# Optimization experiments

Hardware: AMD Instinct MI355X
Metric: run time of the kernel (lower is better)

The kernel has to match this reference:

```python
import jax, jax.numpy as jnp
import numpy as np

D_MODEL = 2048
N_HEADS = 32
N_KV = 8
D_K = D_MODEL // N_HEADS  # 64
N_REP = N_HEADS // N_KV   # 4


def setup_inputs() -> dict:
    key = jax.random.key(0)
    ks = jax.random.split(key, 5)
    B, T = 2, 2048
    s = 0.02
    return {
        "x": jax.random.normal(ks[0], (B, T, D_MODEL), dtype=jnp.float32),
        "Wq": jax.random.normal(ks[1], (D_MODEL, D_MODEL), dtype=jnp.float32) * s,
        "Wk": jax.random.normal(ks[2], (N_KV * D_K, D_MODEL), dtype=jnp.float32) * s,
        "Wv": jax.random.normal(ks[3], (N_KV * D_K, D_MODEL), dtype=jnp.float32) * s,
        "Wo": jax.random.normal(ks[4], (D_MODEL, D_MODEL), dtype=jnp.float32) * s,
    }


def reference(x, Wq, Wk, Wv, Wo):
    B, T, C = x.shape
    # projections (torch Linear: x @ W.T)
    Q = (x @ Wq.T).reshape(B, T, N_KV, N_REP, D_K)  # group query heads by kv group
    K = (x @ Wk.T).reshape(B, T, N_KV, D_K)
    V = (x @ Wv.T).reshape(B, T, N_KV, D_K)
    scale = 1.0 / jnp.sqrt(jnp.asarray(D_K, dtype=x.dtype))
    # scores: (B, n_kv, n_rep, T, T) == repeated-KV scores without materializing repeats
    scores = jnp.einsum('btgrd,bsgd->bgrts', Q, K) * scale
    causal_mask = jnp.triu(jnp.ones((T, T), dtype=bool), k=1)
    scores = jnp.where(causal_mask, -jnp.inf, scores)
    attn = jax.nn.softmax(scores, axis=-1)
    out = jnp.einsum('bgrts,bsgd->btgrd', attn, V).reshape(B, T, C)
    return out @ Wo.T
```

## Files before the change

kernel.cpp:

```cpp
#include <hip/hip_runtime.h>
#include <hip/hip_bf16.h>

typedef __attribute__((ext_vector_type(8))) short bf16x8;
typedef __attribute__((ext_vector_type(4))) float floatx4;

constexpr int D_MODEL = 2048;
constexpr int N_HEADS = 32;
constexpr int N_KV    = 8;
constexpr int B_      = 2;
constexpr int T_      = 2048;
constexpr int BT      = B_ * T_;
constexpr int NQKV    = 3072;

__device__ __forceinline__ unsigned short f2bf(float f) {
    __hip_bfloat16 h = __float2bfloat16(f);
    return *reinterpret_cast<unsigned short*>(&h);
}

__device__ __forceinline__ void gll16(const void* g, void* l) {
    typedef const __attribute__((address_space(1))) unsigned int* gp_t;
    typedef __attribute__((address_space(3))) unsigned int* lp_t;
    __builtin_amdgcn_global_load_lds((gp_t)g, (lp_t)l, 16, 0, 0);
}

__global__ __launch_bounds__(256) void cvt_all(
        const float* __restrict__ x,  const float* __restrict__ wq,
        const float* __restrict__ wk, const float* __restrict__ wv,
        unsigned short* __restrict__ dst) {
    size_t i4 = (size_t)blockIdx.x * 256 + threadIdx.x;
    size_t e = i4 * 4;
    const float* src; size_t off;
    if (e < 8388608)        { src = x;  off = 0; }
    else if (e < 12582912)  { src = wq; off = 8388608; }
    else if (e < 13631488)  { src = wk; off = 12582912; }
    else                    { src = wv; off = 13631488; }
    float4 f = *reinterpret_cast<const float4*>(src + (e - off));
    unsigned short u[4] = {f2bf(f.x), f2bf(f.y), f2bf(f.z), f2bf(f.w)};
    reinterpret_cast<uint2*>(dst)[i4] = *reinterpret_cast<const uint2*>(u);
}

__global__ __launch_bounds__(256) void cvt_bf16(
        const float* __restrict__ src, unsigned short* __restrict__ dst, int n4) {
    int i = blockIdx.x * 256 + threadIdx.x;
    if (i < n4) {
        float4 f = reinterpret_cast<const float4*>(src)[i];
        unsigned short u[4] = {f2bf(f.x), f2bf(f.y), f2bf(f.z), f2bf(f.w)};
        reinterpret_cast<uint2*>(dst)[i] = *reinterpret_cast<const uint2*>(u);
    }
}

template<bool C_F32>
__global__ __launch_bounds__(256) void gemm128(
        const unsigned short* __restrict__ A,
        const unsigned short* __restrict__ Bb,
        void* __restrict__ Cp,
        int M, int N, int K) {
    __shared__ unsigned short As[128 * 64];
    __shared__ unsigned short Bs[128 * 64];
    const int t = threadIdx.x;
    const int wave = t >> 6, lane = t & 63;
    const int l16 = lane & 15, quad = lane >> 4;
    const int wm = (wave & 1) * 64, wn = (wave >> 1) * 64;
    const int mtile = blockIdx.y * 128, ntile = blockIdx.x * 128;

    floatx4 acc[4][4] = {};

    for (int k0 = 0; k0 < K; k0 += 64) {
        __syncthreads();
#pragma unroll
        for (int c = 0; c < 4; c++) {
            int s = (c * 4 + wave) * 64 + lane;
            int row = s >> 3, k8 = (s & 7) ^ (row & 7);
            gll16(&A[(size_t)(mtile + row) * K + k0 + k8 * 8], &As[(c * 4 + wave) * 512]);
            gll16(&Bb[(size_t)(ntile + row) * K + k0 + k8 * 8], &Bs[(c * 4 + wave) * 512]);
        }
        __syncthreads();
#pragma unroll
        for (int kc = 0; kc < 2; kc++) {
            bf16x8 af[4], bfr[4];
#pragma unroll
            for (int i = 0; i < 4; i++) {
                int arow = wm + i * 16 + l16;
                af[i] = *reinterpret_cast<const bf16x8*>(
                    &As[(arow * 8 + ((kc * 4 + quad) ^ (arow & 7))) * 8]);
                int brow = wn + i * 16 + l16;
                bfr[i] = *reinterpret_cast<const bf16x8*>(
                    &Bs[(brow * 8 + ((kc * 4 + quad) ^ (brow & 7))) * 8]);
            }
#pragma unroll
            for (int i = 0; i < 4; i++)
#pragma unroll
                for (int jn = 0; jn < 4; jn++)
                    acc[i][jn] = __builtin_amdgcn_mfma_f32_16x16x32_bf16(
                        af[i], bfr[jn], acc[i][jn], 0, 0, 0);
        }
    }
#pragma unroll
    for (int i = 0; i < 4; i++)
#pragma unroll
        for (int jn = 0; jn < 4; jn++)
#pragma unroll
            for (int r = 0; r < 4; r++) {
                int row = mtile + wm + i * 16 + quad * 4 + r;
                int col = ntile + wn + jn * 16 + l16;
                if constexpr (C_F32)
                    ((float*)Cp)[(size_t)row * N + col] = acc[i][jn][r];
                else
                    ((unsigned short*)Cp)[(size_t)row * N + col] = f2bf(acc[i][jn][r]);
            }
}

__global__ __launch_bounds__(256) void vtrans(
        const unsigned short* __restrict__ QKV,
        unsigned short* __restrict__ Vt) {
    __shared__ unsigned short Ts[64][72];
    const int tb = blockIdx.x * 64;
    const int bg = blockIdx.y;
    const int b = bg >> 3, g = bg & 7;
    const int t = threadIdx.x;
#pragma unroll
    for (int it = 0; it < 2; it++) {
        int row = (t >> 3) + it * 32;
        int sl = t & 7;
        *reinterpret_cast<uint4*>(&Ts[row][sl * 8]) =
            *reinterpret_cast<const uint4*>(
                &QKV[(size_t)(b * T_ + tb + row) * NQKV + 2560 + g * 64 + sl * 8]);
    }
    __syncthreads();
#pragma unroll
    for (int it = 0; it < 2; it++) {
        int d = (t >> 3) + it * 32;
        int ks = t & 7;
        unsigned short u[8];
#pragma unroll
        for (int j = 0; j < 8; j++) u[j] = Ts[ks * 8 + j][d];
        *reinterpret_cast<uint4*>(&Vt[((size_t)bg * 64 + d) * T_ + tb + ks * 8]) =
            *reinterpret_cast<const uint4*>(u);
    }
}

__global__ __launch_bounds__(256) void attn3(
        const unsigned short* __restrict__ QKV,
        const unsigned short* __restrict__ Vt,
        unsigned short* __restrict__ O) {
    __shared__ unsigned short Ks[64 * 64];
    __shared__ unsigned short Vs[64 * 64];
    __shared__ unsigned short Ps[4][16 * 72];
    const int j  = blockIdx.x;
    const int bh = blockIdx.y;
    const int b = bh >> 5, h = bh & 31;
    const int g = h >> 2;
    const int t = threadIdx.x, wave = t >> 6, lane = t & 63;
    const int l16 = lane & 15, quad = lane >> 4;

    const int qtlA = j, qtlB = 31 - j;
    const int qA = qtlA * 64 + wave * 16 + l16;
    const int qB = qtlB * 64 + wave * 16 + l16;

    const unsigned short* qpA = QKV + (size_t)(b * T_ + qA) * NQKV + h * 64;
    const unsigned short* qpB = QKV + (size_t)(b * T_ + qB) * NQKV + h * 64;
    bf16x8 qA0 = *reinterpret_cast<const bf16x8*>(qpA + quad * 8);
    bf16x8 qA1 = *reinterpret_cast<const bf16x8*>(qpA + 32 + quad * 8);
    bf16x8 qB0 = *reinterpret_cast<const bf16x8*>(qpB + quad * 8);
    bf16x8 qB1 = *reinterpret_cast<const bf16x8*>(qpB + 32 + quad * 8);

    floatx4 oA[4] = {}, oB[4] = {};
    float lpA = 0.f, lpB = 0.f;

    for (int kt = 0; kt <= qtlB; kt++) {
        const int kb = kt * 64;
        const bool doA = (kt <= qtlA);
        __syncthreads();
#pragma unroll
        for (int c = 0; c < 2; c++) {
            int s = (c * 4 + wave) * 64 + lane;
            int row = s >> 3, k8 = (s & 7) ^ (row & 7);
            gll16(&QKV[(size_t)(b * T_ + kb + row) * NQKV + 2048 + g * 64 + k8 * 8],
                  &Ks[(c * 4 + wave) * 512]);
            gll16(&Vt[((size_t)(b * 8 + g) * 64 + row) * T_ + kb + k8 * 8],
                  &Vs[(c * 4 + wave) * 512]);
        }
        __syncthreads();

        floatx4 sA[4], sB[4];
#pragma unroll
        for (int nt = 0; nt < 4; nt++) {
            int krow = nt * 16 + l16;
            bf16x8 k0 = *reinterpret_cast<const bf16x8*>(
                &Ks[(krow * 8 + (quad ^ (krow & 7))) * 8]);
            bf16x8 k1 = *reinterpret_cast<const bf16x8*>(
                &Ks[(krow * 8 + ((4 + quad) ^ (krow & 7))) * 8]);
            floatx4 z = {};
            z = __builtin_amdgcn_mfma_f32_16x16x32_bf16(k0, qB0, z, 0, 0, 0);
            sB[nt] = __builtin_amdgcn_mfma_f32_16x16x32_bf16(k1, qB1, z, 0, 0, 0);
            if (doA) {
                floatx4 za = {};
                za = __builtin_amdgcn_mfma_f32_16x16x32_bf16(k0, qA0, za, 0, 0, 0);
                sA[nt] = __builtin_amdgcn_mfma_f32_16x16x32_bf16(k1, qA1, za, 0, 0, 0);
            }
        }

        const bool diagB = (kt == qtlB), diagA = (kt == qtlA);
#pragma unroll
        for (int nt = 0; nt < 4; nt++) {
            unsigned short u[4];
#pragma unroll
            for (int r = 0; r < 4; r++) {
                float p = __expf(sB[nt][r] * 0.125f);
                if (diagB && (kb + nt * 16 + quad * 4 + r) > qB) p = 0.f;
                lpB += p;
                u[r] = f2bf(p);
            }
            *reinterpret_cast<uint2*>(&Ps[wave][l16 * 72 + nt * 16 + quad * 4]) =
                *reinterpret_cast<const uint2*>(u);
        }
        {
            bf16x8 p0 = *reinterpret_cast<const bf16x8*>(&Ps[wave][l16 * 72 + quad * 8]);
            bf16x8 p1 = *reinterpret_cast<const bf16x8*>(&Ps[wave][l16 * 72 + 32 + quad * 8]);
#pragma unroll
            for (int dt = 0; dt < 4; dt++) {
                int vrow = dt * 16 + l16;
                bf16x8 v0 = *reinterpret_cast<const bf16x8*>(
                    &Vs[(vrow * 8 + (quad ^ (vrow & 7))) * 8]);
                bf16x8 v1 = *reinterpret_cast<const bf16x8*>(
                    &Vs[(vrow * 8 + ((4 + quad) ^ (vrow & 7))) * 8]);
                oB[dt] = __builtin_amdgcn_mfma_f32_16x16x32_bf16(p0, v0, oB[dt], 0, 0, 0);
                oB[dt] = __builtin_amdgcn_mfma_f32_16x16x32_bf16(p1, v1, oB[dt], 0, 0, 0);
            }
        }
        if (doA) {
#pragma unroll
            for (int nt = 0; nt < 4; nt++) {
                unsigned short u[4];
#pragma unroll
                for (int r = 0; r < 4; r++) {
                    float p = __expf(sA[nt][r] * 0.125f);
                    if (diagA && (kb + nt * 16 + quad * 4 + r) > qA) p = 0.f;
                    lpA += p;
                    u[r] = f2bf(p);
                }
                *reinterpret_cast<uint2*>(&Ps[wave][l16 * 72 + nt * 16 + quad * 4]) =
                    *reinterpret_cast<const uint2*>(u);
            }
            bf16x8 p0 = *reinterpret_cast<const bf16x8*>(&Ps[wave][l16 * 72 + quad * 8]);
            bf16x8 p1 = *reinterpret_cast<const bf16x8*>(&Ps[wave][l16 * 72 + 32 + quad * 8]);
#pragma unroll
            for (int dt = 0; dt < 4; dt++) {
                int vrow = dt * 16 + l16;
                bf16x8 v0 = *reinterpret_cast<const bf16x8*>(
                    &Vs[(vrow * 8 + (quad ^ (vrow & 7))) * 8]);
                bf16x8 v1 = *reinterpret_cast<const bf16x8*>(
                    &Vs[(vrow * 8 + ((4 + quad) ^ (vrow & 7))) * 8]);
                oA[dt] = __builtin_amdgcn_mfma_f32_16x16x32_bf16(p0, v0, oA[dt], 0, 0, 0);
                oA[dt] = __builtin_amdgcn_mfma_f32_16x16x32_bf16(p1, v1, oA[dt], 0, 0, 0);
            }
        }
    }

    lpA += __shfl_xor(lpA, 16); lpA += __shfl_xor(lpA, 32);
    lpB += __shfl_xor(lpB, 16); lpB += __shfl_xor(lpB, 32);
#pragma unroll
    for (int r = 0; r < 4; r++) {
        float invA = 1.0f / __shfl(lpA, quad * 4 + r);
        float invB = 1.0f / __shfl(lpB, quad * 4 + r);
        int rowA = b * T_ + qtlA * 64 + wave * 16 + quad * 4 + r;
        int rowB = b * T_ + qtlB * 64 + wave * 16 + quad * 4 + r;
#pragma unroll
        for (int dt = 0; dt < 4; dt++) {
            O[(size_t)rowA * D_MODEL + h * 64 + dt * 16 + l16] = f2bf(oA[dt][r] * invA);
            O[(size_t)rowB * D_MODEL + h * 64 + dt * 16 + l16] = f2bf(oB[dt][r] * invB);
        }
    }
}

extern "C" void kernel_launch(void* const* d_in, const int* in_sizes, int n_in,
                              void* d_out, int out_size, void* d_ws, size_t ws_size,
                              hipStream_t stream) {
    const float* x  = (const float*)d_in[0];
    const float* Wq = (const float*)d_in[1];
    const float* Wk = (const float*)d_in[2];
    const float* Wv = (const float*)d_in[3];
    const float* Wo = (const float*)d_in[4];

    unsigned short* xb   = (unsigned short*)d_ws;
    unsigned short* Wqkv = xb + (size_t)BT * D_MODEL;
    unsigned short* QKVo = Wqkv + (size_t)NQKV * D_MODEL;
    unsigned short* Vt   = QKVo + (size_t)BT * NQKV;
    unsigned short* Aw   = xb;
    unsigned short* Wob  = Wqkv;

    dim3 blk(256);
    cvt_all<<<dim3(14336), blk, 0, stream>>>(x, Wq, Wk, Wv, xb);
    gemm128<false><<<dim3(NQKV / 128, BT / 128), blk, 0, stream>>>(
        xb, Wqkv, QKVo, BT, NQKV, D_MODEL);
    cvt_bf16<<<dim3(D_MODEL * D_MODEL / 4 / 256), blk, 0, stream>>>(
        Wo, Wob, D_MODEL * D_MODEL / 4);
    vtrans<<<dim3(T_ / 64, B_ * N_KV), blk, 0, stream>>>(QKVo, Vt);
    attn3<<<dim3(16, B_ * N_HEADS), blk, 0, stream>>>(QKVo, Vt, Aw);
    gemm128<true><<<dim3(D_MODEL / 128, BT / 128), blk, 0, stream>>>(
        Aw, Wob, d_out, BT, D_MODEL, D_MODEL);
}
```

Measured before the change: 314.9 us.

## Fold softmax scale into Q projection, use exp2 and MFMA row sums

The QKV GEMM epilogue now multiplies the Q columns by 0.125*log2(e), so the attention kernel can call exp2 directly without a per-element multiply. The row-sum of probabilities is computed with an MFMA against a ones vector instead of scalar adds and shuffles. The attention loop now processes the two paired query tiles one after the other instead of interleaving them, and the causal mask check is limited to the diagonal tile. This cuts VALU work but loads the K/V tiles twice for the shared early key blocks, and Q is rounded to bf16 after scaling.

```diff
diff --git a/kernel.cpp b/kernel.cpp
--- a/kernel.cpp
+++ b/kernel.cpp
@@ -11,6 +11,8 @@
 constexpr int T_      = 2048;
 constexpr int BT      = B_ * T_;
 constexpr int NQKV    = 3072;
+
+constexpr float Q_SCALE = 0.18033688011112042f;
 
 __device__ __forceinline__ unsigned short f2bf(float f) {
     __hip_bfloat16 h = __float2bfloat16(f);
@@ -49,7 +51,7 @@
     }
 }
 
-template<bool C_F32>
+template<bool C_F32, bool SCALEQ>
 __global__ __launch_bounds__(256) void gemm128(
         const unsigned short* __restrict__ A,
         const unsigned short* __restrict__ Bb,
@@ -95,6 +97,7 @@
                         af[i], bfr[jn], acc[i][jn], 0, 0, 0);
         }
     }
+    float cscale = (SCALEQ && ntile < 2048) ? Q_SCALE : 1.0f;
 #pragma unroll
     for (int i = 0; i < 4; i++)
 #pragma unroll
@@ -106,7 +109,8 @@
                 if constexpr (C_F32)
                     ((float*)Cp)[(size_t)row * N + col] = acc[i][jn][r];
                 else
-                    ((unsigned short*)Cp)[(size_t)row * N + col] = f2bf(acc[i][jn][r]);
+                    ((unsigned short*)Cp)[(size_t)row * N + col] =
+                        f2bf(acc[i][jn][r] * cscale);
             }
 }
 
@@ -139,7 +143,7 @@
     }
 }
 
-__global__ __launch_bounds__(256) void attn3(
+__global__ __launch_bounds__(256) void attn4(
         const unsigned short* __restrict__ QKV,
         const unsigned short* __restrict__ Vt,
         unsigned short* __restrict__ O) {
@@ -153,70 +157,77 @@
     const int t = threadIdx.x, wave = t >> 6, lane = t & 63;
     const int l16 = lane & 15, quad = lane >> 4;
 
-    const int qtlA = j, qtlB = 31 - j;
-    const int qA = qtlA * 64 + wave * 16 + l16;
-    const int qB = qtlB * 64 + wave * 16 + l16;
-
-    const unsigned short* qpA = QKV + (size_t)(b * T_ + qA) * NQKV + h * 64;
-    const unsigned short* qpB = QKV + (size_t)(b * T_ + qB) * NQKV + h * 64;
-    bf16x8 qA0 = *reinterpret_cast<const bf16x8*>(qpA + quad * 8);
-    bf16x8 qA1 = *reinterpret_cast<const bf16x8*>(qpA + 32 + quad * 8);
-    bf16x8 qB0 = *reinterpret_cast<const bf16x8*>(qpB + quad * 8);
-    bf16x8 qB1 = *reinterpret_cast<const bf16x8*>(qpB + 32 + quad * 8);
-
-    floatx4 oA[4] = {}, oB[4] = {};
-    float lpA = 0.f, lpB = 0.f;
-
-    for (int kt = 0; kt <= qtlB; kt++) {
-        const int kb = kt * 64;
-        const bool doA = (kt <= qtlA);
-        __syncthreads();
-#pragma unroll
-        for (int c = 0; c < 2; c++) {
-            int s = (c * 4 + wave) * 64 + lane;
-            int row = s >> 3, k8 = (s & 7) ^ (row & 7);
-            gll16(&QKV[(size_t)(b * T_ + kb + row) * NQKV + 2048 + g * 64 + k8 * 8],
-                  &Ks[(c * 4 + wave) * 512]);
-            gll16(&Vt[((size_t)(b * 8 + g) * 64 + row) * T_ + kb + k8 * 8],
-                  &Vs[(c * 4 + wave) * 512]);
-        }
-        __syncthreads();
-
-        floatx4 sA[4], sB[4];
-#pragma unroll
-        for (int nt = 0; nt < 4; nt++) {
-            int krow = nt * 16 + l16;
-            bf16x8 k0 = *reinterpret_cast<const bf16x8*>(
-                &Ks[(krow * 8 + (quad ^ (krow & 7))) * 8]);
-            bf16x8 k1 = *reinterpret_cast<const bf16x8*>(
-                &Ks[(krow * 8 + ((4 + quad) ^ (krow & 7))) * 8]);
-            floatx4 z = {};
-            z = __builtin_amdgcn_mfma_f32_16x16x32_bf16(k0, qB0, z, 0, 0, 0);
-            sB[nt] = __builtin_amdgcn_mfma_f32_16x16x32_bf16(k1, qB1, z, 0, 0, 0);
-            if (doA) {
-                floatx4 za = {};
-                za = __builtin_amdgcn_mfma_f32_16x16x32_bf16(k0, qA0, za, 0, 0, 0);
-                sA[nt] = __builtin_amdgcn_mfma_f32_16x16x32_bf16(k1, qA1, za, 0, 0, 0);
-            }
-        }
-
-        const bool diagB = (kt == qtlB), diagA = (kt == qtlA);
-#pragma unroll
-        for (int nt = 0; nt < 4; nt++) {
-            unsigned short u[4];
-#pragma unroll
-            for (int r = 0; r < 4; r++) {
-                float p = __expf(sB[nt][r] * 0.125f);
-                if (diagB && (kb + nt * 16 + quad * 4 + r) > qB) p = 0.f;
-                lpB += p;
-                u[r] = f2bf(p);
-            }
-            *reinterpret_cast<uint2*>(&Ps[wave][l16 * 72 + nt * 16 + quad * 4]) =
-                *reinterpret_cast<const uint2*>(u);
-        }
-        {
+    bf16x8 ones;
+#pragma unroll
+    for (int i = 0; i < 8; i++) ones[i] = (short)0x3F80;
+
+    for (int pp = 0; pp < 2; pp++) {
+        const int qtl = pp ? (31 - j) : j;
+        const int qb0 = qtl * 64;
+        const int qq = qb0 + wave * 16 + l16;
+        const unsigned short* qptr = QKV + (size_t)(b * T_ + qq) * NQKV + h * 64;
+        bf16x8 qf0 = *reinterpret_cast<const bf16x8*>(qptr + quad * 8);
+        bf16x8 qf1 = *reinterpret_cast<const bf16x8*>(qptr + 32 + quad * 8);
+
+        floatx4 o[4] = {};
+        floatx4 lacc = {};
+
+        for (int kt = 0; kt <= qtl; kt++) {
+            const int kb = kt * 64;
+            __syncthreads();
+#pragma unroll
+            for (int c = 0; c < 2; c++) {
+                int s = (c * 4 + wave) * 64 + lane;
+                int row = s >> 3, k8 = (s & 7) ^ (row & 7);
+                gll16(&QKV[(size_t)(b * T_ + kb + row) * NQKV + 2048 + g * 64 + k8 * 8],
+                      &Ks[(c * 4 + wave) * 512]);
+                gll16(&Vt[((size_t)(b * 8 + g) * 64 + row) * T_ + kb + k8 * 8],
+                      &Vs[(c * 4 + wave) * 512]);
+            }
+            __syncthreads();
+
+            floatx4 sT[4];
+#pragma unroll
+            for (int nt = 0; nt < 4; nt++) {
+                int krow = nt * 16 + l16;
+                bf16x8 k0 = *reinterpret_cast<const bf16x8*>(
+                    &Ks[(krow * 8 + (quad ^ (krow & 7))) * 8]);
+                bf16x8 k1 = *reinterpret_cast<const bf16x8*>(
+                    &Ks[(krow * 8 + ((4 + quad) ^ (krow & 7))) * 8]);
+                floatx4 z = {};
+                z = __builtin_amdgcn_mfma_f32_16x16x32_bf16(k0, qf0, z, 0, 0, 0);
+                sT[nt] = __builtin_amdgcn_mfma_f32_16x16x32_bf16(k1, qf1, z, 0, 0, 0);
+            }
+
+            if (kt == qtl) {
+#pragma unroll
+                for (int nt = 0; nt < 4; nt++) {
+                    unsigned short u[4];
+#pragma unroll
+                    for (int r = 0; r < 4; r++) {
+                        float p = __builtin_amdgcn_exp2f(sT[nt][r]);
+                        if ((kb + nt * 16 + quad * 4 + r) > qq) p = 0.f;
+                        u[r] = f2bf(p);
+                    }
+                    *reinterpret_cast<uint2*>(&Ps[wave][l16 * 72 + nt * 16 + quad * 4]) =
+                        *reinterpret_cast<const uint2*>(u);
+                }
+            } else {
+#pragma unroll
+                for (int nt = 0; nt < 4; nt++) {
+                    unsigned short u[4];
+#pragma unroll
+                    for (int r = 0; r < 4; r++)
+                        u[r] = f2bf(__builtin_amdgcn_exp2f(sT[nt][r]));
+                    *reinterpret_cast<uint2*>(&Ps[wave][l16 * 72 + nt * 16 + quad * 4]) =
+                        *reinterpret_cast<const uint2*>(u);
+                }
+            }
+
             bf16x8 p0 = *reinterpret_cast<const bf16x8*>(&Ps[wave][l16 * 72 + quad * 8]);
             bf16x8 p1 = *reinterpret_cast<const bf16x8*>(&Ps[wave][l16 * 72 + 32 + quad * 8]);
+            lacc = __builtin_amdgcn_mfma_f32_16x16x32_bf16(p0, ones, lacc, 0, 0, 0);
+            lacc = __builtin_amdgcn_mfma_f32_16x16x32_bf16(p1, ones, lacc, 0, 0, 0);
 #pragma unroll
             for (int dt = 0; dt < 4; dt++) {
                 int vrow = dt * 16 + l16;
@@ -224,51 +235,18 @@
                     &Vs[(vrow * 8 + (quad ^ (vrow & 7))) * 8]);
                 bf16x8 v1 = *reinterpret_cast<const bf16x8*>(
                     &Vs[(vrow * 8 + ((4 + quad) ^ (vrow & 7))) * 8]);
-                oB[dt] = __builtin_amdgcn_mfma_f32_16x16x32_bf16(p0, v0, oB[dt], 0, 0, 0);
-                oB[dt] = __builtin_amdgcn_mfma_f32_16x16x32_bf16(p1, v1, oB[dt], 0, 0, 0);
-            }
-        }
-        if (doA) {
-#pragma unroll
-            for (int nt = 0; nt < 4; nt++) {
-                unsigned short u[4];
-#pragma unroll
-                for (int r = 0; r < 4; r++) {
-                    float p = __expf(sA[nt][r] * 0.125f);
-                    if (diagA && (kb + nt * 16 + quad * 4 + r) > qA) p = 0.f;
-                    lpA += p;
-                    u[r] = f2bf(p);
-                }
-                *reinterpret_cast<uint2*>(&Ps[wave][l16 * 72 + nt * 16 + quad * 4]) =
-                    *reinterpret_cast<const uint2*>(u);
-            }
-            bf16x8 p0 = *reinterpret_cast<const bf16x8*>(&Ps[wave][l16 * 72 + quad * 8]);
-            bf16x8 p1 = *reinterpret_cast<const bf16x8*>(&Ps[wave][l16 * 72 + 32 + quad * 8]);
-#pragma unroll
-            for (int dt = 0; dt < 4; dt++) {
-                int vrow = dt * 16 + l16;
-                bf16x8 v0 = *reinterpret_cast<const bf16x8*>(
-                    &Vs[(vrow * 8 + (quad ^ (vrow & 7))) * 8]);
-                bf16x8 v1 = *reinterpret_cast<const bf16x8*>(
-                    &Vs[(vrow * 8 + ((4 + quad) ^ (vrow & 7))) * 8]);
-                oA[dt] = __builtin_amdgcn_mfma_f32_16x16x32_bf16(p0, v0, oA[dt], 0, 0, 0);
-                oA[dt] = __builtin_amdgcn_mfma_f32_16x16x32_bf16(p1, v1, oA[dt], 0, 0, 0);
-            }
-        }
-    }
-
-    lpA += __shfl_xor(lpA, 16); lpA += __shfl_xor(lpA, 32);
-    lpB += __shfl_xor(lpB, 16); lpB += __shfl_xor(lpB, 32);
-#pragma unroll
-    for (int r = 0; r < 4; r++) {
-        float invA = 1.0f / __shfl(lpA, quad * 4 + r);
-        float invB = 1.0f / __shfl(lpB, quad * 4 + r);
-        int rowA = b * T_ + qtlA * 64 + wave * 16 + quad * 4 + r;
-        int rowB = b * T_ + qtlB * 64 + wave * 16 + quad * 4 + r;
-#pragma unroll
-        for (int dt = 0; dt < 4; dt++) {
-            O[(size_t)rowA * D_MODEL + h * 64 + dt * 16 + l16] = f2bf(oA[dt][r] * invA);
-            O[(size_t)rowB * D_MODEL + h * 64 + dt * 16 + l16] = f2bf(oB[dt][r] * invB);
+                o[dt] = __builtin_amdgcn_mfma_f32_16x16x32_bf16(p0, v0, o[dt], 0, 0, 0);
+                o[dt] = __builtin_amdgcn_mfma_f32_16x16x32_bf16(p1, v1, o[dt], 0, 0, 0);
+            }
+        }
+
+#pragma unroll
+        for (int r = 0; r < 4; r++) {
+            float inv = 1.0f / lacc[r];
+            int row = b * T_ + qb0 + wave * 16 + quad * 4 + r;
+#pragma unroll
+            for (int dt = 0; dt < 4; dt++)
+                O[(size_t)row * D_MODEL + h * 64 + dt * 16 + l16] = f2bf(o[dt][r] * inv);
         }
     }
 }
@@ -291,12 +269,12 @@
 
     dim3 blk(256);
     cvt_all<<<dim3(14336), blk, 0, stream>>>(x, Wq, Wk, Wv, xb);
-    gemm128<false><<<dim3(NQKV / 128, BT / 128), blk, 0, stream>>>(
+    gemm128<false, true><<<dim3(NQKV / 128, BT / 128), blk, 0, stream>>>(
         xb, Wqkv, QKVo, BT, NQKV, D_MODEL);
     cvt_bf16<<<dim3(D_MODEL * D_MODEL / 4 / 256), blk, 0, stream>>>(
         Wo, Wob, D_MODEL * D_MODEL / 4);
     vtrans<<<dim3(T_ / 64, B_ * N_KV), blk, 0, stream>>>(QKVo, Vt);
-    attn3<<<dim3(16, B_ * N_HEADS), blk, 0, stream>>>(QKVo, Vt, Aw);
-    gemm128<true><<<dim3(D_MODEL / 128, BT / 128), blk, 0, stream>>>(
+    attn4<<<dim3(16, B_ * N_HEADS), blk, 0, stream>>>(QKVo, Vt, Aw);
+    gemm128<true, false><<<dim3(D_MODEL / 128, BT / 128), blk, 0, stream>>>(
         Aw, Wob, d_out, BT, D_MODEL, D_MODEL);
 }
```

Result: faster. 288.0 us (-8.6%).
